# Performance work log

Measured on AMD Instinct MI355X. Metric: run time of the kernel, lower is better.

## Reference

```python
import jax, jax.numpy as jnp
import numpy as np

NEG_INF = -1e30  # large negative in fp32; rows always have >=1 allowed entry (causal diagonal)


def setup_inputs() -> dict:
    key = jax.random.key(0)
    k0, k1, k2, k3 = jax.random.split(key, 4)
    b, s, nh, hs = 2, 2048, 16, 64
    q = jax.random.normal(k0, (b, s, nh, hs), dtype=jnp.float32)
    k = jax.random.normal(k1, (b, s, nh, hs), dtype=jnp.float32)
    v = jax.random.normal(k2, (b, s, nh, hs), dtype=jnp.float32)
    # per-batch GLM break point: prefix [0, bp) is bidirectional, rest is causal
    glm_mask = jax.random.randint(k3, (b,), 0, s).astype(jnp.int32)
    return {"q": q, "k": k, "v": v, "glm_mask": glm_mask}


def reference(q, k, v, glm_mask):
    # q: [b, s_q, nh, hs]; k, v: [b, s_k, nh, hs]; glm_mask: [b] int32 break points
    b, s_q, nh, hs = q.shape
    s_k = k.shape[1]
    scale = 1.0 / np.sqrt(hs)  # softmax_scale default 1/sqrt(head_dim)

    # attention scores [b, nh, s_q, s_k]
    scores = jnp.einsum("bqhd,bkhd->bhqk", q, k) * scale

    # GLM mask: position i may attend to j iff (j <= i) [causal] or (j < break_point) [bidirectional prefix]
    qi = jnp.arange(s_q)[:, None]          # [s_q, 1]
    kj = jnp.arange(s_k)[None, :]          # [1, s_k]
    causal = kj <= qi                       # [s_q, s_k]
    prefix = jnp.arange(s_k)[None, :] < glm_mask[:, None]  # [b, s_k]
    allowed = causal[None, :, :] | prefix[:, None, :]       # [b, s_q, s_k]

    scores = jnp.where(allowed[:, None, :, :], scores, NEG_INF)
    p = jax.nn.softmax(scores, axis=-1)     # [b, nh, s_q, s_k]
    out = jnp.einsum("bhqk,bkhd->bqhd", p, v)  # [b, s_q, nh, hs]
    return out
```

## Files before the change

### kernel.cpp

```cpp
#include <hip/hip_runtime.h>
#include <hip/hip_bf16.h>


typedef __attribute__((ext_vector_type(8))) __bf16 bf16x8;
typedef __attribute__((ext_vector_type(4))) __bf16 bf16x4;
typedef __attribute__((ext_vector_type(4))) float floatx4;

#define S_LEN 2048
#define NH 16
#define HS 64
#define RS 1024
#define KB_ELEMS (2 * NH * S_LEN * HS)
#define SCALE_LOG2E 0.18033688011112042f

#if __has_builtin(__builtin_amdgcn_exp2f)
#define EXP2(x) __builtin_amdgcn_exp2f(x)
#else
#define EXP2(x) exp2f(x)
#endif

#define MFMA(a, b, c) __builtin_amdgcn_mfma_f32_16x16x32_bf16(a, b, c, 0, 0, 0)

#define GLOAD16(GP, LP)                                                        \
  __builtin_amdgcn_global_load_lds(                                            \
      (const __attribute__((address_space(1))) void*)(GP),                     \
      (__attribute__((address_space(3))) void*)(LP), 16, 0, 0)

__global__ __launch_bounds__(256) void conv_kv(const float* __restrict__ k,
                                               const float* __restrict__ v,
                                               __bf16* __restrict__ kbuf,
                                               __bf16* __restrict__ vbuf)
{
    __shared__ __align__(16) __bf16 tile[64][72];
    const int tid = threadIdx.x;

    const int bh = blockIdx.x >> 5;
    const int st = blockIdx.x & 31;
    const int b = bh >> 4, h = bh & 15;
    const int s0 = st * 64;

#pragma unroll
    for (int it = 0; it < 4; ++it) {
        const int idx = it * 256 + tid;
        const int s = idx >> 4, f4 = idx & 15;
        floatx4 val = *(const floatx4*)(k + ((size_t)(b * 2048 + s0 + s)) * 1024 + h * 64 + f4 * 4);
        bf16x4 w;
        w[0] = (__bf16)(val[0] * SCALE_LOG2E); w[1] = (__bf16)(val[1] * SCALE_LOG2E);
        w[2] = (__bf16)(val[2] * SCALE_LOG2E); w[3] = (__bf16)(val[3] * SCALE_LOG2E);
        *(bf16x4*)(kbuf + ((size_t)((b * 16 + h) * 2048 + s0 + s)) * 64 + f4 * 4) = w;
    }

#pragma unroll
    for (int it = 0; it < 4; ++it) {
        const int idx = it * 256 + tid;
        const int s = idx >> 4, f4 = idx & 15;
        floatx4 val = *(const floatx4*)(v + ((size_t)(b * 2048 + s0 + s)) * 1024 + h * 64 + f4 * 4);
#pragma unroll
        for (int i = 0; i < 4; ++i)
            tile[f4 * 4 + i][s] = (__bf16)val[i];
    }
    __syncthreads();
#pragma unroll
    for (int it = 0; it < 2; ++it) {
        const int idx = it * 256 + tid;
        const int d = idx >> 3, sg = idx & 7;
        bf16x8 w = *(const bf16x8*)&tile[d][sg * 8];
        *(bf16x8*)(vbuf + ((size_t)((b * 16 + h) * 64 + d)) * 2048 + s0 + sg * 8) = w;
    }
}

__global__ __launch_bounds__(64, 1) void fa_part10(
    const float* __restrict__ q, const __bf16* __restrict__ kb,
    const __bf16* __restrict__ vt, const int* __restrict__ glm_mask,
    float* __restrict__ out)
{
    __shared__ __align__(16) __bf16 ldsK[2][64 * 64];
    __shared__ __align__(16) __bf16 ldsV[2][64 * 64];
    __shared__ __align__(16) __bf16 pt[2][2][16 * 40];

    const int lane = threadIdx.x;
    const int col  = lane & 15, quad = lane >> 4;

    const int tile = blockIdx.x >> 5;
    const int head = blockIdx.x & 31;
    const int b = head >> 4, h = head & 15;
    const int q0 = (63 - tile) * 32;

    const int bp = glm_mask[b];
    int klen = q0 + 32; if (bp > klen) klen = bp;
    const int nch = (klen + 63) >> 6;

    const __bf16* kbh = kb + ((size_t)(b * 16 + h)) * (2048 * 64);
    const __bf16* vth = vt + ((size_t)(b * 16 + h)) * (64 * 2048);
    const size_t obase = (size_t)b * (S_LEN * RS) + h * HS;

    const int rowi = lane >> 3;
    const int gswz = ((lane & 7) ^ rowi) << 4;

#define STAGE_CHUNK(K0, NB)                                                    \
  {                                                                            \
    const char* gk = (const char*)kbh + (size_t)(K0) * 128;                    \
    const char* gv = (const char*)vth + (size_t)(K0) * 2;                      \
    _Pragma("unroll")                                                          \
    for (int i = 0; i < 8; ++i) {                                              \
      GLOAD16(gk + (size_t)(i * 8 + rowi) * 128 + gswz, &ldsK[NB][i * 512]);   \
      GLOAD16(gv + (size_t)(i * 8 + rowi) * 4096 + gswz, &ldsV[NB][i * 512]);  \
    }                                                                          \
  }

    bf16x8 aq[2][2];
#pragma unroll
    for (int rg = 0; rg < 2; ++rg) {
        const float* qp = q + obase + (size_t)(q0 + rg * 16 + col) * RS + quad * 8;
        floatx4 a0 = *(const floatx4*)qp;
        floatx4 a1 = *(const floatx4*)(qp + 4);
        floatx4 a2 = *(const floatx4*)(qp + 32);
        floatx4 a3 = *(const floatx4*)(qp + 36);
#pragma unroll
        for (int i = 0; i < 4; ++i) {
            aq[rg][0][i] = (__bf16)a0[i]; aq[rg][0][4 + i] = (__bf16)a1[i];
            aq[rg][1][i] = (__bf16)a2[i]; aq[rg][1][4 + i] = (__bf16)a3[i];
        }
    }

    floatx4 o[2][4];
    float ls[2][4];
#pragma unroll
    for (int rg = 0; rg < 2; ++rg)
#pragma unroll
        for (int f = 0; f < 4; ++f) {
            o[rg][f] = (floatx4){0.f, 0.f, 0.f, 0.f};
            ls[rg][f] = 0.f;
        }

    STAGE_CHUNK(0, 0);

    const int cswz = (col & 7) << 4;

    for (int c = 0; c < nch; ++c) {
        const int k0 = c * 64;
        const int cur = c & 1;

        __asm__ __volatile__("s_waitcnt vmcnt(0)" ::: "memory");

        const char* lK = (const char*)&ldsK[cur][0];
        const char* lV = (const char*)&ldsV[cur][0];
        bf16x8 bk[4][2], bv[4][2];
#pragma unroll
        for (int kg = 0; kg < 4; ++kg)
#pragma unroll
            for (int hf = 0; hf < 2; ++hf)
                bk[kg][hf] = *(const bf16x8*)(lK + (kg * 16 + col) * 128 + ((hf * 64 + quad * 16) ^ cswz));
#pragma unroll
        for (int f = 0; f < 4; ++f)
#pragma unroll
            for (int kh = 0; kh < 2; ++kh)
                bv[f][kh] = *(const bf16x8*)(lV + (f * 16 + col) * 128 + ((kh * 64 + quad * 16) ^ cswz));

        if (c + 1 < nch)
            STAGE_CHUNK(k0 + 64, cur ^ 1);

        floatx4 z = {0.f, 0.f, 0.f, 0.f};
        floatx4 s[2][4];
        __builtin_amdgcn_s_setprio(1);
#pragma unroll
        for (int rg = 0; rg < 2; ++rg)
#pragma unroll
            for (int kg = 0; kg < 4; ++kg) {
                s[rg][kg] = MFMA(aq[rg][0], bk[kg][0], z);
                s[rg][kg] = MFMA(aq[rg][1], bk[kg][1], s[rg][kg]);
            }
        __builtin_amdgcn_s_setprio(0);

#pragma unroll
        for (int kh = 0; kh < 2; ++kh) {
#pragma unroll
            for (int rg = 0; rg < 2; ++rg) {
                __bf16* pw = &pt[kh][rg][0];
#pragma unroll
                for (int g2 = 0; g2 < 2; ++g2) {
                    const int kj = k0 + (kh * 2 + g2) * 16 + col;
                    const bool pre = kj < bp;
#pragma unroll
                    for (int r = 0; r < 4; ++r) {
                        const int qi = q0 + rg * 16 + quad * 4 + r;
                        float e = EXP2(s[rg][kh * 2 + g2][r]);
                        float p = (pre || (kj <= qi)) ? e : 0.f;
                        ls[rg][r] += p;
                        pw[(quad * 4 + r) * 40 + g2 * 16 + col] = (__bf16)p;
                    }
                }
            }
        }
        __asm__ __volatile__("" ::: "memory");
        __builtin_amdgcn_s_waitcnt(0xC07F);
        __asm__ __volatile__("" ::: "memory");

        __builtin_amdgcn_s_setprio(1);
#pragma unroll
        for (int kh = 0; kh < 2; ++kh)
#pragma unroll
            for (int rg = 0; rg < 2; ++rg) {
                bf16x8 ap = *(const bf16x8*)(&pt[kh][rg][0] + col * 40 + quad * 8);
#pragma unroll
                for (int f = 0; f < 4; ++f)
                    o[rg][f] = MFMA(ap, bv[f][kh], o[rg][f]);
            }
        __builtin_amdgcn_s_setprio(0);
        __asm__ __volatile__("" ::: "memory");
    }

#pragma unroll
    for (int rg = 0; rg < 2; ++rg)
#pragma unroll
        for (int r = 0; r < 4; ++r) {
            float l = ls[rg][r];
            l += __shfl_xor(l, 1);
            l += __shfl_xor(l, 2);
            l += __shfl_xor(l, 4);
            l += __shfl_xor(l, 8);
            const float inv = (l > 0.f) ? (1.f / l) : 0.f;
            const int row = q0 + rg * 16 + quad * 4 + r;
            float* op = out + obase + (size_t)row * RS;
#pragma unroll
            for (int f = 0; f < 4; ++f)
                op[f * 16 + col] = o[rg][f][r] * inv;
        }
}

extern "C" void kernel_launch(void* const* d_in, const int* in_sizes, int n_in,
                              void* d_out, int out_size, void* d_ws, size_t ws_size,
                              hipStream_t stream) {
    const float* q = (const float*)d_in[0];
    const float* k = (const float*)d_in[1];
    const float* v = (const float*)d_in[2];
    const int* glm = (const int*)d_in[3];
    float* out     = (float*)d_out;

    const size_t kb_bytes = (size_t)KB_ELEMS * 2;
    __bf16* kbuf = (__bf16*)d_ws;
    __bf16* vbuf = (__bf16*)((char*)d_ws + kb_bytes);

    hipLaunchKernelGGL(conv_kv, dim3(1024), dim3(256), 0, stream,
                       k, v, kbuf, vbuf);
    hipLaunchKernelGGL(fa_part10, dim3(2048), dim3(64), 0, stream,
                       q, kbuf, vbuf, glm, out);
}
```

Baseline: 174.1 us.

## Load V directly into registers, split PV pass, skip masking on full chunks

V fragments are now fetched straight from global memory into registers with inline global_load_dwordx4, and V is no longer staged through LDS, which roughly halves LDS use. The exp/write and PV MFMA work is split into two half-passes with explicit vmcnt/lgkmcnt waits so the MFMAs can start before all loads land. Chunks that are fully unmasked skip the per-element mask test, and launch bounds allow two blocks per CU. The trade-off is that V loads sit on the critical path without LDS staging, and the hand-written waitcnt counts must stay in step with the loads actually issued.

New measurement: 161.8 us. 7.1% less time.

```diff
diff --git a/kernel.cpp b/kernel.cpp
--- a/kernel.cpp
+++ b/kernel.cpp
@@ -69,14 +69,13 @@
     }
 }
 
-__global__ __launch_bounds__(64, 1) void fa_part10(
+__global__ __launch_bounds__(64, 2) void fa_part12(
     const float* __restrict__ q, const __bf16* __restrict__ kb,
     const __bf16* __restrict__ vt, const int* __restrict__ glm_mask,
     float* __restrict__ out)
 {
     __shared__ __align__(16) __bf16 ldsK[2][64 * 64];
-    __shared__ __align__(16) __bf16 ldsV[2][64 * 64];
-    __shared__ __align__(16) __bf16 pt[2][2][16 * 40];
+    __shared__ __align__(16) __bf16 pt[2][16 * 40];
 
     const int lane = threadIdx.x;
     const int col  = lane & 15, quad = lane >> 4;
@@ -97,16 +96,16 @@
     const int rowi = lane >> 3;
     const int gswz = ((lane & 7) ^ rowi) << 4;
 
-#define STAGE_CHUNK(K0, NB)                                                    \
+#define STAGE_K(K0, NB)                                                        \
   {                                                                            \
     const char* gk = (const char*)kbh + (size_t)(K0) * 128;                    \
-    const char* gv = (const char*)vth + (size_t)(K0) * 2;                      \
     _Pragma("unroll")                                                          \
-    for (int i = 0; i < 8; ++i) {                                              \
+    for (int i = 0; i < 8; ++i)                                                \
       GLOAD16(gk + (size_t)(i * 8 + rowi) * 128 + gswz, &ldsK[NB][i * 512]);   \
-      GLOAD16(gv + (size_t)(i * 8 + rowi) * 4096 + gswz, &ldsV[NB][i * 512]);  \
-    }                                                                          \
   }
+
+    const unsigned long long vlane =
+        (unsigned long long)((const char*)vth + (size_t)col * 4096 + quad * 16);
 
     bf16x8 aq[2][2];
 #pragma unroll
@@ -133,9 +132,44 @@
             ls[rg][f] = 0.f;
         }
 
-    STAGE_CHUNK(0, 0);
+    STAGE_K(0, 0);
 
     const int cswz = (col & 7) << 4;
+
+#define EXP_WRITE(KH)                                                          \
+  _Pragma("unroll")                                                            \
+  for (int rg = 0; rg < 2; ++rg) {                                             \
+    __bf16* pw = &pt[rg][0];                                                   \
+    _Pragma("unroll")                                                          \
+    for (int g2 = 0; g2 < 2; ++g2) {                                           \
+      const int kj = k0 + ((KH) * 2 + g2) * 16 + col;                          \
+      const bool pre = kj < bp;                                                \
+      _Pragma("unroll")                                                        \
+      for (int r = 0; r < 4; ++r) {                                            \
+        float e = EXP2(s[rg][(KH) * 2 + g2][r]);                               \
+        if (!full) {                                                           \
+          const int qi = q0 + rg * 16 + quad * 4 + r;                          \
+          if (!(pre || (kj <= qi))) e = 0.f;                                   \
+        }                                                                      \
+        ls[rg][r] += e;                                                        \
+        pw[(quad * 4 + r) * 40 + g2 * 16 + col] = (__bf16)e;                   \
+      }                                                                        \
+    }                                                                          \
+  }
+
+#define PV_PASS(KH)                                                            \
+  {                                                                            \
+    __builtin_amdgcn_s_setprio(1);                                             \
+    _Pragma("unroll")                                                          \
+    for (int rg = 0; rg < 2; ++rg) {                                           \
+      bf16x8 ap = *(const bf16x8*)(&pt[rg][0] + col * 40 + quad * 8);          \
+      _Pragma("unroll")                                                        \
+      for (int f = 0; f < 4; ++f)                                              \
+        o[rg][f] = MFMA(ap, __builtin_bit_cast(bf16x8, bvr[f][KH]), o[rg][f]); \
+    }                                                                          \
+    __builtin_amdgcn_s_setprio(0);                                             \
+    __asm__ __volatile__("" ::: "memory");  \
+  }
 
     for (int c = 0; c < nch; ++c) {
         const int k0 = c * 64;
@@ -143,22 +177,26 @@
 
         __asm__ __volatile__("s_waitcnt vmcnt(0)" ::: "memory");
 
+        floatx4 bvr[4][2];
+#pragma unroll
+        for (int f = 0; f < 4; ++f)
+#pragma unroll
+            for (int kh = 0; kh < 2; ++kh) {
+                unsigned long long va = vlane + (size_t)k0 * 2 + f * 65536 + kh * 64;
+                __asm__ __volatile__("global_load_dwordx4 %0, %1, off"
+                                     : "=v"(bvr[f][kh]) : "v"(va) : "memory");
+            }
+
         const char* lK = (const char*)&ldsK[cur][0];
-        const char* lV = (const char*)&ldsV[cur][0];
-        bf16x8 bk[4][2], bv[4][2];
+        bf16x8 bk[4][2];
 #pragma unroll
         for (int kg = 0; kg < 4; ++kg)
 #pragma unroll
             for (int hf = 0; hf < 2; ++hf)
                 bk[kg][hf] = *(const bf16x8*)(lK + (kg * 16 + col) * 128 + ((hf * 64 + quad * 16) ^ cswz));
-#pragma unroll
-        for (int f = 0; f < 4; ++f)
-#pragma unroll
-            for (int kh = 0; kh < 2; ++kh)
-                bv[f][kh] = *(const bf16x8*)(lV + (f * 16 + col) * 128 + ((kh * 64 + quad * 16) ^ cswz));
 
         if (c + 1 < nch)
-            STAGE_CHUNK(k0 + 64, cur ^ 1);
+            STAGE_K(k0 + 64, cur ^ 1);
 
         floatx4 z = {0.f, 0.f, 0.f, 0.f};
         floatx4 s[2][4];
@@ -172,42 +210,21 @@
             }
         __builtin_amdgcn_s_setprio(0);
 
-#pragma unroll
-        for (int kh = 0; kh < 2; ++kh) {
-#pragma unroll
-            for (int rg = 0; rg < 2; ++rg) {
-                __bf16* pw = &pt[kh][rg][0];
-#pragma unroll
-                for (int g2 = 0; g2 < 2; ++g2) {
-                    const int kj = k0 + (kh * 2 + g2) * 16 + col;
-                    const bool pre = kj < bp;
-#pragma unroll
-                    for (int r = 0; r < 4; ++r) {
-                        const int qi = q0 + rg * 16 + quad * 4 + r;
-                        float e = EXP2(s[rg][kh * 2 + g2][r]);
-                        float p = (pre || (kj <= qi)) ? e : 0.f;
-                        ls[rg][r] += p;
-                        pw[(quad * 4 + r) * 40 + g2 * 16 + col] = (__bf16)p;
-                    }
-                }
-            }
-        }
-        __asm__ __volatile__("" ::: "memory");
-        __builtin_amdgcn_s_waitcnt(0xC07F);
-        __asm__ __volatile__("" ::: "memory");
-
-        __builtin_amdgcn_s_setprio(1);
-#pragma unroll
-        for (int kh = 0; kh < 2; ++kh)
-#pragma unroll
-            for (int rg = 0; rg < 2; ++rg) {
-                bf16x8 ap = *(const bf16x8*)(&pt[kh][rg][0] + col * 40 + quad * 8);
-#pragma unroll
-                for (int f = 0; f < 4; ++f)
-                    o[rg][f] = MFMA(ap, bv[f][kh], o[rg][f]);
-            }
-        __builtin_amdgcn_s_setprio(0);
-        __asm__ __volatile__("" ::: "memory");
+        const bool full = (k0 + 63 < bp) || (k0 + 63 <= q0);
+
+        EXP_WRITE(0);
+        if (c + 1 < nch) {
+            __asm__ __volatile__("s_waitcnt vmcnt(8) lgkmcnt(0)" ::: "memory");
+        } else {
+            __asm__ __volatile__("s_waitcnt vmcnt(0) lgkmcnt(0)" ::: "memory");
+        }
+        __builtin_amdgcn_sched_barrier(0);
+        PV_PASS(0);
+
+        EXP_WRITE(1);
+        __asm__ __volatile__("s_waitcnt lgkmcnt(0)" ::: "memory");
+        __builtin_amdgcn_sched_barrier(0);
+        PV_PASS(1);
     }
 
 #pragma unroll
@@ -243,6 +260,6 @@
 
     hipLaunchKernelGGL(conv_kv, dim3(1024), dim3(256), 0, stream,
                        k, v, kbuf, vbuf);
-    hipLaunchKernelGGL(fa_part10, dim3(2048), dim3(64), 0, stream,
+    hipLaunchKernelGGL(fa_part12, dim3(2048), dim3(64), 0, stream,
                        q, kbuf, vbuf, glm, out);
 }
```
